# Performance work log

Measured on AMD Instinct MI355X. Metric: run time of the kernel, lower is better.

Reference implementation:

```python
import jax, jax.numpy as jnp
import numpy as np

B, M, N_STYLE, K, F = 4, 8192, 8192, 8, 288


def _graphconv(x, src, dst, W, b, num_nodes):
    # DGL GraphConv, norm='both': h_v = (sum_{u->v} x_u * d_out(u)^-1/2) * d_in(v)^-1/2 @ W + b
    ones = jnp.ones(src.shape[0], x.dtype)
    deg_out = jnp.clip(jax.ops.segment_sum(ones, src, num_segments=num_nodes), 1.0)
    deg_in = jnp.clip(jax.ops.segment_sum(ones, dst, num_segments=num_nodes), 1.0)
    h = x * (deg_out ** -0.5)[:, None]                      # [N, F] src-normalized
    agg = jax.ops.segment_sum(h[src], dst, num_segments=num_nodes)  # gather+scatter-add
    agg = agg * (deg_in ** -0.5)[:, None]
    return agg @ W + b


def setup_inputs() -> dict:
    key = jax.random.key(0)
    ks = jax.random.split(key, 8)
    return {
        "feat_c": jax.random.normal(ks[0], (B, M, F), jnp.float32),
        "feat_s": jax.random.normal(ks[1], (B, N_STYLE, F), jnp.float32),
        "idx_k1": jax.random.randint(ks[2], (B, M, K), 0, N_STYLE, dtype=jnp.int32),
        "idx_k2": jax.random.randint(ks[3], (B, M, K), 0, M, dtype=jnp.int32),
        "W1": jax.random.normal(ks[4], (F, F), jnp.float32) * (1.0 / np.sqrt(F)),
        "b1": jnp.zeros((F,), jnp.float32),
        "W2": jax.random.normal(ks[5], (F, F), jnp.float32) * (1.0 / np.sqrt(F)),
        "b2": jnp.zeros((F,), jnp.float32),
    }


def reference(feat_c, feat_s, idx_k1, idx_k2, W1, b1, W2, b2):
    b, m, f = feat_c.shape
    n = feat_s.shape[1]
    k = idx_k1.shape[2]
    num_nodes = m + n
    # idx_v: range(m).view(1,m,1).expand(2,m,k).view(-1)
    idx_v = jnp.tile(jnp.repeat(jnp.arange(m, dtype=jnp.int32), k), 2)  # [2*m*k]
    # idx_u: cat((idx_k2, idx_k1 + m), dim=1).view(b, -1)
    idx_u = jnp.concatenate([idx_k2, idx_k1 + m], axis=1).reshape(b, -1)  # [b, 2*m*k]
    feat = jnp.concatenate([feat_c, feat_s], axis=1)  # [b, m+n, f]

    def per_graph(x, src):
        h = _graphconv(x, src, idx_v, W1, b1, num_nodes)
        h = jax.nn.relu(h)
        h = _graphconv(h, src, idx_v, W2, b2, num_nodes)
        return h[:m]  # [m, f]

    return jax.vmap(per_graph)(feat, idx_u)  # [b, m, f]
```

## Files before the change

### kernel.cpp

```cpp
#include <hip/hip_runtime.h>

#define B 4
#define M 8192
#define NSTY 8192
#define KNB 8
#define F 288
#define NT (M + NSTY)
#define BM (B * M)

typedef __attribute__((ext_vector_type(8))) short short8;
typedef __attribute__((ext_vector_type(4))) float floatx4;
typedef __attribute__((ext_vector_type(2))) float floatx2;

__device__ __forceinline__ float u2f(unsigned int u) {
    union { unsigned int u; float f; } c; c.u = u; return c.f;
}
__device__ __forceinline__ unsigned short f2b(float x) {
    union { float f; unsigned int u; } c; c.f = x;
    unsigned int r = c.u + 0x7FFFu + ((c.u >> 16) & 1u);
    return (unsigned short)(r >> 16);
}
__device__ __forceinline__ floatx2 bpair(unsigned int p) {
    floatx2 r;
    r.x = u2f(p << 16);
    r.y = u2f(p & 0xFFFF0000u);
    return r;
}
__device__ __forceinline__ void gload_lds16(const void* g, void* l) {
    __builtin_amdgcn_global_load_lds(
        (const __attribute__((address_space(1))) unsigned int*)g,
        (__attribute__((address_space(3))) unsigned int*)l, 16, 0, 0);
}

#define PREP_DEG   1024
#define PREP_CVT   18432
#define PREP_PKW   648
__global__ void prep_kernel(const int* __restrict__ idx_k1, const int* __restrict__ idx_k2,
                            int* __restrict__ deg,
                            const float* __restrict__ fc, const float* __restrict__ fs,
                            unsigned short* __restrict__ fb,
                            const float* __restrict__ W1, const float* __restrict__ W2,
                            unsigned short* __restrict__ Wp1, unsigned short* __restrict__ Wp2) {
    int blk = blockIdx.x;
    if (blk < PREP_DEG) {
        int t = blk * 256 + threadIdx.x;
        int b = t / (M * KNB);
        atomicAdd(&deg[b * NT + idx_k2[t]], 1);
        atomicAdd(&deg[b * NT + M + idx_k1[t]], 1);
    } else if (blk < PREP_DEG + PREP_CVT) {
        unsigned int t = (unsigned int)(blk - PREP_DEG) * 256 + threadIdx.x;
        unsigned int e = t * 4;
        int row = (int)(e / F);
        int f = (int)(e - (unsigned int)row * F);
        int b = row >> 14, v = row & (NT - 1);
        const float* src = (v < M) ? fc + ((size_t)b * M + v) * F + f
                                   : fs + ((size_t)b * NSTY + (v - M)) * F + f;
        float4 x = *(const float4*)src;
        uint2 o;
        o.x = (unsigned int)f2b(x.x) | ((unsigned int)f2b(x.y) << 16);
        o.y = (unsigned int)f2b(x.z) | ((unsigned int)f2b(x.w) << 16);
        *(uint2*)(fb + e) = o;
    } else {
        int t = (blk - PREP_DEG - PREP_CVT) * 256 + threadIdx.x;
        if (t >= 2 * F * F) return;
        int half = t >= F * F;
        int tt = t - half * F * F;
        int k = tt / F, n = tt - k * F;
        const float* W = half ? W2 : W1;
        unsigned short* Wp = half ? Wp2 : Wp1;
        Wp[((size_t)(k >> 3) * F + n) * 8 + (k & 7)] = f2b(W[tt]);
    }
}

template<int LAYER>
__global__ void agg_kernel(const unsigned short* __restrict__ src_tbl,
                           const int* __restrict__ idx_k1, const int* __restrict__ idx_k2,
                           const int* __restrict__ deg, const float* __restrict__ b1,
                           unsigned short* __restrict__ aggb) {
    int wid = threadIdx.x >> 6, lane = threadIdx.x & 63;
    int blk = blockIdx.x;
    int rx = blk & 7;
    int b = rx >> 1;
    int sub = (blk >> 3) * 2 + (rx & 1);
    int r = sub * 4 + wid;
    size_t ebase = ((size_t)b * M + r) * KNB;

    int u = 0; float w = 0.f;
    if (lane < 8) {
        u = idx_k2[ebase + lane];
        int d = deg[b * NT + u];
        w = rsqrtf((float)(d < 1 ? 1 : d));
    } else if (lane < 16) {
        u = M + idx_k1[ebase + lane - 8];
        int d = deg[b * NT + u];
        w = rsqrtf((float)(d < 1 ? 1 : d));
    }

    floatx2 a0[2] = {{0.f,0.f},{0.f,0.f}};
    floatx2 a1[2] = {{0.f,0.f},{0.f,0.f}};
    if (LAYER == 2) {
        float S = 0.f;
        #pragma unroll
        for (int k = 8; k < 16; ++k) S += __shfl(w, k);
        float4 t4 = *(const float4*)(b1 + 4 * lane);
        a0[0].x = fmaxf(t4.x, 0.f) * S; a0[0].y = fmaxf(t4.y, 0.f) * S;
        a0[1].x = fmaxf(t4.z, 0.f) * S; a0[1].y = fmaxf(t4.w, 0.f) * S;
        if (lane < 8) {
            float4 t5 = *(const float4*)(b1 + 256 + 4 * lane);
            a1[0].x = fmaxf(t5.x, 0.f) * S; a1[0].y = fmaxf(t5.y, 0.f) * S;
            a1[1].x = fmaxf(t5.z, 0.f) * S; a1[1].y = fmaxf(t5.w, 0.f) * S;
        }
    }

    const unsigned short* base = src_tbl + (size_t)b * (LAYER == 1 ? NT : M) * F;
    #pragma unroll
    for (int k = 0; k < ((LAYER == 1) ? 16 : 8); ++k) {
        int   uk = __shfl(u, k);
        float wk = __shfl(w, k);
        floatx2 wk2 = {wk, wk};
        const unsigned short* s = base + (size_t)uk * F;
        uint2 d0 = *(const uint2*)(s + 4 * lane);
        a0[0] += wk2 * bpair(d0.x);
        a0[1] += wk2 * bpair(d0.y);
        if (lane < 8) {
            uint2 d1 = *(const uint2*)(s + 256 + 4 * lane);
            a1[0] += wk2 * bpair(d1.x);
            a1[1] += wk2 * bpair(d1.y);
        }
    }

    unsigned short* dst = aggb + ((size_t)b * M + r) * F;
    uint2 o;
    o.x = (unsigned int)f2b(a0[0].x * 0.25f) | ((unsigned int)f2b(a0[0].y * 0.25f) << 16);
    o.y = (unsigned int)f2b(a0[1].x * 0.25f) | ((unsigned int)f2b(a0[1].y * 0.25f) << 16);
    *(uint2*)(dst + 4 * lane) = o;
    if (lane < 8) {
        uint2 o1;
        o1.x = (unsigned int)f2b(a1[0].x * 0.25f) | ((unsigned int)f2b(a1[0].y * 0.25f) << 16);
        o1.y = (unsigned int)f2b(a1[1].x * 0.25f) | ((unsigned int)f2b(a1[1].y * 0.25f) << 16);
        *(uint2*)(dst + 256 + 4 * lane) = o1;
    }
}

template<int RELU, int OUTBF16>
__global__ __launch_bounds__(256, 2) void gemm_kernel(
        const unsigned short* __restrict__ A,
        const unsigned short* __restrict__ Wp,
        const float* __restrict__ bias,
        void* __restrict__ Cout) {
    __shared__ __align__(16) unsigned short sA[64 * F];
    __shared__ __align__(16) unsigned short sB[2][4 * F * 8];
    int tid = threadIdx.x;
    int wid = tid >> 6, lane = tid & 63;
    int wm = wid & 1, wn = wid >> 1;
    int quad = lane >> 4, r16 = lane & 15;
    int blk = blockIdx.x;
    int rx = blk & 7;
    int b = rx >> 1;
    int sub = (blk >> 3) * 2 + (rx & 1);
    int row0 = b * M + sub * 64;

    const unsigned short* Ab = A + (size_t)row0 * F;
    #pragma unroll
    for (int rr = 0; rr < 9; ++rr)
        gload_lds16(Ab + (rr * 256 + tid) * 8, &sA[(rr * 256 + tid) * 8]);
    if (tid < 128) {
        #pragma unroll
        for (int rr = 0; rr < 9; ++rr)
            gload_lds16(Wp + (rr * 128 + tid) * 8, &sB[0][(rr * 128 + tid) * 8]);
    }

    floatx4 acc[9][2];
    #pragma unroll
    for (int ct = 0; ct < 9; ++ct)
        #pragma unroll
        for (int rt = 0; rt < 2; ++rt)
            acc[ct][rt] = (floatx4){0.f, 0.f, 0.f, 0.f};

    __syncthreads();

    for (int s = 0; s < 9; ++s) {
        if (s < 8 && tid < 128) {
            const unsigned short* src = Wp + (size_t)(s + 1) * 4 * F * 8;
            unsigned short* dstb = sB[(s + 1) & 1];
            #pragma unroll
            for (int rr = 0; rr < 9; ++rr)
                gload_lds16(src + (rr * 128 + tid) * 8, dstb + (rr * 128 + tid) * 8);
        }
        short8 a0 = *(const short8*)&sA[(wm * 32 + r16) * F + s * 32 + quad * 8];
        short8 a1 = *(const short8*)&sA[(wm * 32 + 16 + r16) * F + s * 32 + quad * 8];
        const unsigned short* bb = &sB[s & 1][(quad * F + wn * 144 + r16) * 8];
        #pragma unroll
        for (int ct = 0; ct < 9; ++ct) {
            short8 bf = *(const short8*)(bb + ct * 128);
            acc[ct][0] = __builtin_amdgcn_mfma_f32_16x16x32_bf16(a0, bf, acc[ct][0], 0, 0, 0);
            acc[ct][1] = __builtin_amdgcn_mfma_f32_16x16x32_bf16(a1, bf, acc[ct][1], 0, 0, 0);
        }
        __syncthreads();
    }

    #pragma unroll
    for (int ct = 0; ct < 9; ++ct) {
        int col = wn * 144 + ct * 16 + r16;
        float bc = bias[col];
        #pragma unroll
        for (int rt = 0; rt < 2; ++rt) {
            #pragma unroll
            for (int rg = 0; rg < 4; ++rg) {
                float v = acc[ct][rt][rg] + bc;
                if (RELU) v = fmaxf(v, 0.f);
                int grow = row0 + wm * 32 + quad * 4 + rt * 16 + rg;
                if (OUTBF16) ((unsigned short*)Cout)[(size_t)grow * F + col] = f2b(v);
                else         ((float*)Cout)[(size_t)grow * F + col] = v;
            }
        }
    }
}

extern "C" void kernel_launch(void* const* d_in, const int* in_sizes, int n_in,
                              void* d_out, int out_size, void* d_ws, size_t ws_size,
                              hipStream_t stream) {
    const float* feat_c = (const float*)d_in[0];
    const float* feat_s = (const float*)d_in[1];
    const int*   idx_k1 = (const int*)d_in[2];
    const int*   idx_k2 = (const int*)d_in[3];
    const float* W1     = (const float*)d_in[4];
    const float* b1     = (const float*)d_in[5];
    const float* W2     = (const float*)d_in[6];
    const float* b2     = (const float*)d_in[7];

    char* ws = (char*)d_ws;
    int*            deg  = (int*)ws;
    unsigned short* Wp1  = (unsigned short*)(ws + 262144);
    unsigned short* Wp2  = (unsigned short*)(ws + 262144 + 165888);
    unsigned short* aggb = (unsigned short*)(ws + 262144 + 2 * 165888);

    unsigned short* featb = (unsigned short*)d_out;
    unsigned short* h1b   = (unsigned short*)d_out;
    float*          out   = (float*)d_out;

    hipMemsetAsync(deg, 0, (size_t)B * NT * sizeof(int), stream);
    prep_kernel<<<PREP_DEG + PREP_CVT + PREP_PKW, 256, 0, stream>>>(
        idx_k1, idx_k2, deg, feat_c, feat_s, featb, W1, W2, Wp1, Wp2);

    agg_kernel<1><<<BM / 4, 256, 0, stream>>>(featb, idx_k1, idx_k2, deg, b1, aggb);
    gemm_kernel<1, 1><<<BM / 64, 256, 0, stream>>>(aggb, Wp1, b1, (void*)h1b);

    agg_kernel<2><<<BM / 4, 256, 0, stream>>>(h1b, idx_k1, idx_k2, deg, b1, aggb);
    gemm_kernel<0, 0><<<BM / 64, 256, 0, stream>>>(aggb, Wp2, b2, (void*)out);
}
```

Baseline: 254.2 us.

## Restructure aggregation kernel: 4 rows per wave, 16-byte gathers batched

The aggregation kernel now processes four destination rows per wavefront instead of one. Each lane loads 16 bytes (8 bf16) of a row, so a 288-wide row is covered by 36 lanes, and the eight neighbor row loads per chunk are issued together before accumulation to raise memory-level parallelism. Index and degree lookups are spread across all 64 lanes, one edge per lane, and the grid shrinks fourfold. The trade-off is that 28 of 64 lanes stay idle during the gather and register pressure rises from holding eight uint4 loads.

```diff
diff --git a/kernel.cpp b/kernel.cpp
--- a/kernel.cpp
+++ b/kernel.cpp
@@ -73,72 +73,88 @@
 }
 
 template<int LAYER>
-__global__ void agg_kernel(const unsigned short* __restrict__ src_tbl,
-                           const int* __restrict__ idx_k1, const int* __restrict__ idx_k2,
-                           const int* __restrict__ deg, const float* __restrict__ b1,
-                           unsigned short* __restrict__ aggb) {
-    int wid = threadIdx.x >> 6, lane = threadIdx.x & 63;
+__global__ __launch_bounds__(256) void agg_kernel(
+        const unsigned short* __restrict__ src_tbl,
+        const int* __restrict__ idx_k1, const int* __restrict__ idx_k2,
+        const int* __restrict__ deg, const float* __restrict__ b1,
+        unsigned short* __restrict__ aggb) {
+    const int NK = (LAYER == 1) ? 16 : 8;
+    int tid = threadIdx.x, wid = tid >> 6, lane = tid & 63;
     int blk = blockIdx.x;
     int rx = blk & 7;
     int b = rx >> 1;
     int sub = (blk >> 3) * 2 + (rx & 1);
-    int r = sub * 4 + wid;
-    size_t ebase = ((size_t)b * M + r) * KNB;
-
-    int u = 0; float w = 0.f;
-    if (lane < 8) {
-        u = idx_k2[ebase + lane];
-        int d = deg[b * NT + u];
-        w = rsqrtf((float)(d < 1 ? 1 : d));
-    } else if (lane < 16) {
-        u = M + idx_k1[ebase + lane - 8];
-        int d = deg[b * NT + u];
-        w = rsqrtf((float)(d < 1 ? 1 : d));
-    }
-
-    floatx2 a0[2] = {{0.f,0.f},{0.f,0.f}};
-    floatx2 a1[2] = {{0.f,0.f},{0.f,0.f}};
-    if (LAYER == 2) {
-        float S = 0.f;
-        #pragma unroll
-        for (int k = 8; k < 16; ++k) S += __shfl(w, k);
-        float4 t4 = *(const float4*)(b1 + 4 * lane);
-        a0[0].x = fmaxf(t4.x, 0.f) * S; a0[0].y = fmaxf(t4.y, 0.f) * S;
-        a0[1].x = fmaxf(t4.z, 0.f) * S; a0[1].y = fmaxf(t4.w, 0.f) * S;
-        if (lane < 8) {
-            float4 t5 = *(const float4*)(b1 + 256 + 4 * lane);
-            a1[0].x = fmaxf(t5.x, 0.f) * S; a1[0].y = fmaxf(t5.y, 0.f) * S;
-            a1[1].x = fmaxf(t5.z, 0.f) * S; a1[1].y = fmaxf(t5.w, 0.f) * S;
-        }
+    int rbase = sub * 16 + wid * 4;
+
+    int i4 = lane >> 4, e = lane & 15;
+    {
+        size_t eb = ((size_t)b * M + rbase + i4) * KNB;
+    }
+    size_t eb = ((size_t)b * M + rbase + i4) * KNB;
+    int u;
+    if (e < 8) u = idx_k2[eb + e];
+    else       u = M + idx_k1[eb + e - 8];
+    int dg = deg[b * NT + u];
+    float w = rsqrtf((float)(dg < 1 ? 1 : dg));
+    float wst = (e >= 8) ? w : 0.f;
+
+    float bb[8];
+    if (LAYER == 2 && lane < 36) {
+        float4 t0 = *(const float4*)(b1 + 8 * lane);
+        float4 t1 = *(const float4*)(b1 + 8 * lane + 4);
+        bb[0]=fmaxf(t0.x,0.f); bb[1]=fmaxf(t0.y,0.f); bb[2]=fmaxf(t0.z,0.f); bb[3]=fmaxf(t0.w,0.f);
+        bb[4]=fmaxf(t1.x,0.f); bb[5]=fmaxf(t1.y,0.f); bb[6]=fmaxf(t1.z,0.f); bb[7]=fmaxf(t1.w,0.f);
     }
 
     const unsigned short* base = src_tbl + (size_t)b * (LAYER == 1 ? NT : M) * F;
-    #pragma unroll
-    for (int k = 0; k < ((LAYER == 1) ? 16 : 8); ++k) {
-        int   uk = __shfl(u, k);
-        float wk = __shfl(w, k);
-        floatx2 wk2 = {wk, wk};
-        const unsigned short* s = base + (size_t)uk * F;
-        uint2 d0 = *(const uint2*)(s + 4 * lane);
-        a0[0] += wk2 * bpair(d0.x);
-        a0[1] += wk2 * bpair(d0.y);
-        if (lane < 8) {
-            uint2 d1 = *(const uint2*)(s + 256 + 4 * lane);
-            a1[0] += wk2 * bpair(d1.x);
-            a1[1] += wk2 * bpair(d1.y);
-        }
-    }
-
-    unsigned short* dst = aggb + ((size_t)b * M + r) * F;
-    uint2 o;
-    o.x = (unsigned int)f2b(a0[0].x * 0.25f) | ((unsigned int)f2b(a0[0].y * 0.25f) << 16);
-    o.y = (unsigned int)f2b(a0[1].x * 0.25f) | ((unsigned int)f2b(a0[1].y * 0.25f) << 16);
-    *(uint2*)(dst + 4 * lane) = o;
-    if (lane < 8) {
-        uint2 o1;
-        o1.x = (unsigned int)f2b(a1[0].x * 0.25f) | ((unsigned int)f2b(a1[0].y * 0.25f) << 16);
-        o1.y = (unsigned int)f2b(a1[1].x * 0.25f) | ((unsigned int)f2b(a1[1].y * 0.25f) << 16);
-        *(uint2*)(dst + 256 + 4 * lane) = o1;
+    unsigned short* dbase = aggb + ((size_t)b * M + rbase) * F;
+
+    #pragma unroll
+    for (int i = 0; i < 4; ++i) {
+        floatx2 acc[4];
+        if (LAYER == 2) {
+            float S = 0.f;
+            #pragma unroll
+            for (int j = 8; j < 16; ++j) S += __shfl(wst, i * 16 + j);
+            #pragma unroll
+            for (int j = 0; j < 4; ++j) { acc[j].x = bb[2*j] * S; acc[j].y = bb[2*j+1] * S; }
+        } else {
+            #pragma unroll
+            for (int j = 0; j < 4; ++j) acc[j] = (floatx2){0.f, 0.f};
+        }
+
+        #pragma unroll
+        for (int c = 0; c < NK / 8; ++c) {
+            const unsigned short* sp[8];
+            #pragma unroll
+            for (int k = 0; k < 8; ++k) {
+                int uk = __shfl(u, i * 16 + c * 8 + k);
+                sp[k] = base + (size_t)uk * F + 8 * lane;
+            }
+            uint4 v[8];
+            if (lane < 36) {
+                #pragma unroll
+                for (int k = 0; k < 8; ++k) v[k] = *(const uint4*)sp[k];
+            }
+            #pragma unroll
+            for (int k = 0; k < 8; ++k) {
+                float wk = __shfl(w, i * 16 + c * 8 + k);
+                floatx2 wk2 = {wk, wk};
+                acc[0] += wk2 * bpair(v[k].x);
+                acc[1] += wk2 * bpair(v[k].y);
+                acc[2] += wk2 * bpair(v[k].z);
+                acc[3] += wk2 * bpair(v[k].w);
+            }
+        }
+
+        if (lane < 36) {
+            uint4 o;
+            o.x = (unsigned int)f2b(acc[0].x*0.25f) | ((unsigned int)f2b(acc[0].y*0.25f) << 16);
+            o.y = (unsigned int)f2b(acc[1].x*0.25f) | ((unsigned int)f2b(acc[1].y*0.25f) << 16);
+            o.z = (unsigned int)f2b(acc[2].x*0.25f) | ((unsigned int)f2b(acc[2].y*0.25f) << 16);
+            o.w = (unsigned int)f2b(acc[3].x*0.25f) | ((unsigned int)f2b(acc[3].y*0.25f) << 16);
+            *(uint4*)(dbase + (size_t)i * F + 8 * lane) = o;
+        }
     }
 }
 
@@ -189,10 +205,10 @@
         }
         short8 a0 = *(const short8*)&sA[(wm * 32 + r16) * F + s * 32 + quad * 8];
         short8 a1 = *(const short8*)&sA[(wm * 32 + 16 + r16) * F + s * 32 + quad * 8];
-        const unsigned short* bb = &sB[s & 1][(quad * F + wn * 144 + r16) * 8];
+        const unsigned short* bbp = &sB[s & 1][(quad * F + wn * 144 + r16) * 8];
         #pragma unroll
         for (int ct = 0; ct < 9; ++ct) {
-            short8 bf = *(const short8*)(bb + ct * 128);
+            short8 bf = *(const short8*)(bbp + ct * 128);
             acc[ct][0] = __builtin_amdgcn_mfma_f32_16x16x32_bf16(a0, bf, acc[ct][0], 0, 0, 0);
             acc[ct][1] = __builtin_amdgcn_mfma_f32_16x16x32_bf16(a1, bf, acc[ct][1], 0, 0, 0);
         }
@@ -243,9 +259,9 @@
     prep_kernel<<<PREP_DEG + PREP_CVT + PREP_PKW, 256, 0, stream>>>(
         idx_k1, idx_k2, deg, feat_c, feat_s, featb, W1, W2, Wp1, Wp2);
 
-    agg_kernel<1><<<BM / 4, 256, 0, stream>>>(featb, idx_k1, idx_k2, deg, b1, aggb);
+    agg_kernel<1><<<BM / 16, 256, 0, stream>>>(featb, idx_k1, idx_k2, deg, b1, aggb);
     gemm_kernel<1, 1><<<BM / 64, 256, 0, stream>>>(aggb, Wp1, b1, (void*)h1b);
 
-    agg_kernel<2><<<BM / 4, 256, 0, stream>>>(h1b, idx_k1, idx_k2, deg, b1, aggb);
+    agg_kernel<2><<<BM / 16, 256, 0, stream>>>(h1b, idx_k1, idx_k2, deg, b1, aggb);
     gemm_kernel<0, 0><<<BM / 64, 256, 0, stream>>>(aggb, Wp2, b2, (void*)out);
 }
```

Result: faster. 230.0 us (-9.5%).
